# Kernel tuning notes

Measured on AMD Instinct MI355X. Metric: run time of the kernel, lower is better.

Reference implementation:

```python
import jax, jax.numpy as jnp
import numpy as np

B, C, D, H, W = 16, 8, 511, 16, 16
NHEADS = 16
DIM = C * H * W          # 2048 hidden size
SEQ = D + 1              # 512 tokens incl. cls
HEAD_DIM = DIM // NHEADS # 128


def setup_inputs() -> dict:
    key = jax.random.key(0)
    ks = jax.random.split(key, 8)
    s = 0.02  # weight init scale
    return {
        "x": jax.random.normal(ks[0], (B, C, D, H, W), jnp.float32),
        "pos_embedding": jax.random.normal(ks[1], (1, SEQ, DIM), jnp.float32),
        "cls": jax.random.normal(ks[2], (1, 1, DIM), jnp.float32),
        "qkv_w": jax.random.normal(ks[3], (DIM, 3 * DIM), jnp.float32) * s,
        "qkv_b": jnp.zeros((3 * DIM,), jnp.float32),
        "proj_w": jax.random.normal(ks[4], (DIM, DIM), jnp.float32) * s,
        "proj_b": jnp.zeros((DIM,), jnp.float32),
    }


def reference(x, pos_embedding, cls, qkv_w, qkv_b, proj_w, proj_b):
    b = x.shape[0]
    # rearrange 'b c d h w -> b d (c h w)'
    tok = jnp.transpose(x, (0, 2, 1, 3, 4)).reshape(b, D, DIM)
    tok = jnp.concatenate([jnp.broadcast_to(cls, (b, 1, DIM)), tok], axis=1)
    tok = tok + pos_embedding  # (b, SEQ, DIM)
    # qkv projection (dropout probs are 0 -> identity)
    qkv = tok @ qkv_w + qkv_b  # (b, SEQ, 3*DIM)
    qkv = qkv.reshape(b, SEQ, 3, NHEADS, HEAD_DIM).transpose(2, 0, 3, 1, 4)
    q, k, v = qkv[0], qkv[1], qkv[2]  # each (b, nH, SEQ, hd)
    scale = HEAD_DIM ** -0.5
    score = jax.nn.softmax(jnp.einsum('bhqd,bhkd->bhqk', q, k) * scale, axis=-1)
    out = jnp.einsum('bhqk,bhkd->bhqd', score, v)
    out = out.transpose(0, 2, 1, 3).reshape(b, SEQ, DIM)
    out = out @ proj_w + proj_b
    return out[:, 0]  # cls token, (b, DIM)
```

## Files before the change

### kernel.cpp

```cpp
#include <hip/hip_runtime.h>


#define BB   16
#define CC   8
#define DD   511
#define DIM  2048
#define SEQ  512
#define NH   16
#define HD   128
#define W3   6144
#define SCALE 0.08838834764831845f

#define Q_OFF   0
#define AO_OFF  2048
#define R_OFF   34816
#define G_OFF   67584
#define SC_OFF  67600
#define U8_OFF  198672

typedef __attribute__((ext_vector_type(8))) short short8;
typedef __attribute__((ext_vector_type(4))) float floatx4;

static __device__ inline short f2bf(float f) {
  union { float f; unsigned u; } v; v.f = f;
  unsigned r = v.u + 0x7fffu + ((v.u >> 16) & 1u);
  return (short)(r >> 16);
}
static __device__ inline float bf2f(short s) {
  union { unsigned u; float f; } v;
  v.u = ((unsigned)(unsigned short)s) << 16;
  return v.f;
}

__global__ __launch_bounds__(256) void k1_q(
    const float* __restrict__ pos, const float* __restrict__ cls,
    const float* __restrict__ qkv_w, const float* __restrict__ qkv_b,
    float* __restrict__ ws) {
  int n  = blockIdx.x * 256 + threadIdx.x;
  int d0 = blockIdx.y * 32;
  float acc = (blockIdx.y == 0) ? qkv_b[n] : 0.f;
#pragma unroll 8
  for (int d = d0; d < d0 + 32; ++d) {
    float t0 = cls[d] + pos[d];
    acc += t0 * qkv_w[(size_t)d * W3 + n];
  }
  atomicAdd(&ws[Q_OFF + n], acc);
}

__global__ __launch_bounds__(256) void k2_r(
    const float* __restrict__ qkv_w, float* __restrict__ ws) {
  __shared__ float qs[64];
  int h = blockIdx.y, ec = blockIdx.z;
  int d = blockIdx.x * 256 + threadIdx.x;
  if (threadIdx.x < 64) qs[threadIdx.x] = ws[Q_OFF + h * HD + ec * 64 + threadIdx.x];
  __syncthreads();
  const float4* w4 = reinterpret_cast<const float4*>(
      qkv_w + (size_t)d * W3 + DIM + h * HD + ec * 64);
  float acc = 0.f;
#pragma unroll
  for (int e4 = 0; e4 < 16; ++e4) {
    float4 w = w4[e4];
    acc += qs[e4*4+0]*w.x + qs[e4*4+1]*w.y + qs[e4*4+2]*w.z + qs[e4*4+3]*w.w;
  }
  atomicAdd(&ws[R_OFF + h * DIM + d], acc * SCALE);
}

__global__ __launch_bounds__(256) void k2b_gamma(
    const float* __restrict__ pos, const float* __restrict__ cls,
    float* __restrict__ ws) {
  __shared__ float red[256];
  int h = blockIdx.x, t = threadIdx.x;
  float part = 0.f;
  for (int d = t; d < DIM; d += 256)
    part += (cls[d] + pos[d]) * ws[R_OFF + h * DIM + d];
  red[t] = part;
  __syncthreads();
  for (int s = 128; s > 0; s >>= 1) {
    if (t < s) red[t] += red[t + s];
    __syncthreads();
  }
  if (t == 0) ws[G_OFF + h] = red[0];
}

__global__ __launch_bounds__(256) void k2c_rbf(float* __restrict__ ws) {
  int i = blockIdx.x * 256 + threadIdx.x;
  float v = ws[R_OFF + i];
  short hi = f2bf(v);
  short lo = f2bf(v - bf2f(hi));
  short* rb = (short*)(ws + U8_OFF);
  rb[i] = hi;
  rb[NH * DIM + i] = lo;
}

__global__ __launch_bounds__(64) void k3_scores_mfma(
    const float* __restrict__ x, const float* __restrict__ pos,
    float* __restrict__ ws) {
  int jt = blockIdx.x, b = blockIdx.y, ks = blockIdx.z;
  int l  = threadIdx.x;
  int m  = l & 15;
  int kg = l >> 4;
  int jrow = 1 + jt * 16 + m;
  int jc = jrow < SEQ ? jrow : (SEQ - 1);
  const size_t xrow = (size_t)b * CC * DD * 256 + (size_t)(jc - 1) * 256;
  const short* rh = (const short*)(ws + U8_OFF);
  const short* rl = rh + NH * DIM;
  floatx4 acc = {0.f, 0.f, 0.f, 0.f};
#pragma unroll 2
  for (int kk = ks * 32; kk < ks * 32 + 32; ++kk) {
    int d0 = kk * 32 + kg * 8;
    int c = d0 >> 8, doff = d0 & 255;
    const float4* xp = reinterpret_cast<const float4*>(
        x + xrow + (size_t)c * DD * 256 + doff);
    const float4* pp = reinterpret_cast<const float4*>(
        pos + (size_t)jc * DIM + d0);
    float4 xa = xp[0], xb = xp[1];
    float4 pa = pp[0], pb = pp[1];
    float f[8] = {xa.x + pa.x, xa.y + pa.y, xa.z + pa.z, xa.w + pa.w,
                  xb.x + pb.x, xb.y + pb.y, xb.z + pb.z, xb.w + pb.w};
    short8 ahi, alo;
#pragma unroll
    for (int i = 0; i < 8; ++i) {
      short hi = f2bf(f[i]);
      ahi[i] = hi;
      alo[i] = f2bf(f[i] - bf2f(hi));
    }
    short8 bhi = *reinterpret_cast<const short8*>(rh + m * DIM + d0);
    short8 blo = *reinterpret_cast<const short8*>(rl + m * DIM + d0);
    acc = __builtin_amdgcn_mfma_f32_16x16x32_bf16(ahi, bhi, acc, 0, 0, 0);
    acc = __builtin_amdgcn_mfma_f32_16x16x32_bf16(ahi, blo, acc, 0, 0, 0);
    acc = __builtin_amdgcn_mfma_f32_16x16x32_bf16(alo, bhi, acc, 0, 0, 0);
  }
  int h = m;
#pragma unroll
  for (int reg = 0; reg < 4; ++reg) {
    int row = kg * 4 + reg;
    int j = 1 + jt * 16 + row;
    if (j < SEQ)
      atomicAdd(&ws[SC_OFF + (size_t)(b * NH + h) * SEQ + j], acc[reg]);
  }
}

__global__ __launch_bounds__(256) void k4_softmax(float* __restrict__ ws) {
  int h = blockIdx.x, b = blockIdx.y, t = threadIdx.x;
  float* sc = ws + SC_OFF + (size_t)(b * NH + h) * SEQ;
  __shared__ float red[256];
  float s0 = (t == 0) ? ws[G_OFF + h] : sc[t];
  float s1 = sc[t + 256];
  red[t] = fmaxf(s0, s1);
  __syncthreads();
  for (int s = 128; s > 0; s >>= 1) { if (t < s) red[t] = fmaxf(red[t], red[t + s]); __syncthreads(); }
  float m = red[0];
  __syncthreads();
  float e0 = __expf(s0 - m), e1 = __expf(s1 - m);
  red[t] = e0 + e1;
  __syncthreads();
  for (int s = 128; s > 0; s >>= 1) { if (t < s) red[t] += red[t + s]; __syncthreads(); }
  float inv = 1.f / red[0];
  sc[t] = e0 * inv;
  sc[t + 256] = e1 * inv;
}

__global__ __launch_bounds__(256) void k5_u(
    const float* __restrict__ x, const float* __restrict__ pos,
    const float* __restrict__ cls, float* __restrict__ ws) {
  int c = blockIdx.x, qc = blockIdx.y, b = blockIdx.z, t = threadIdx.x;
  int d = c * 256 + t;
  __shared__ float pl[NH][64];
  __shared__ float pl0[NH];
  const float* pp = ws + SC_OFF + (size_t)b * NH * SEQ;
  int j0 = 1 + qc * 64;
  for (int i = t; i < NH * 64; i += 256) {
    int h = i >> 6, jj = i & 63;
    int j = j0 + jj;
    pl[h][jj] = (j < SEQ) ? pp[h * SEQ + j] : 0.f;
  }
  if (t < NH) pl0[t] = pp[t * SEQ];
  __syncthreads();
  float acc[NH];
  if (qc == 0) {
    float t0 = cls[d] + pos[d];
#pragma unroll
    for (int h = 0; h < NH; ++h) acc[h] = pl0[h] * t0;
  } else {
#pragma unroll
    for (int h = 0; h < NH; ++h) acc[h] = 0.f;
  }
  const size_t xb = (size_t)b * CC * DD * 256 + (size_t)c * DD * 256 + t;
  const float* posc = pos + c * 256 + t;
#pragma unroll 2
  for (int jt = 0; jt < 64; jt += 4) {
    float xvv[4];
#pragma unroll
    for (int jj = 0; jj < 4; ++jj) {
      int j = j0 + jt + jj;
      xvv[jj] = (j < SEQ)
          ? x[xb + (size_t)(j - 1) * 256] + posc[(size_t)j * DIM]
          : 0.f;
    }
#pragma unroll
    for (int h = 0; h < NH; ++h) {
      float4 p4 = *reinterpret_cast<const float4*>(&pl[h][jt]);
      acc[h] += p4.x * xvv[0] + p4.y * xvv[1] + p4.z * xvv[2] + p4.w * xvv[3];
    }
  }
  float* u = ws + U8_OFF + (size_t)((qc * BB + b) * NH) * DIM + d;
#pragma unroll
  for (int h = 0; h < NH; ++h) u[(size_t)h * DIM] = acc[h];
}

__global__ __launch_bounds__(256) void k6_ao(
    const float* __restrict__ qkv_w, const float* __restrict__ qkv_b,
    float* __restrict__ ws) {
  int nt = blockIdx.x, dc = blockIdx.y, t = threadIdx.x;
  int m = nt * 256 + t;
  int h0 = nt * 2;
  int d0 = dc * 64;
  __shared__ float us[2][64][20];
  for (int i = t; i < 2 * 64 * BB; i += 256) {
    int dd = i & 63, b = (i >> 6) & 15, hh = i >> 10;
    float s = 0.f;
#pragma unroll
    for (int q = 0; q < 8; ++q)
      s += ws[U8_OFF + (size_t)((q * BB + b) * NH + h0 + hh) * DIM + d0 + dd];
    us[hh][dd][b] = s;
  }
  __syncthreads();
  int hl = t >> 7;
  float acc[BB];
#pragma unroll
  for (int b = 0; b < BB; ++b) acc[b] = 0.f;
  const float* wcol = qkv_w + (size_t)d0 * W3 + 2 * DIM + m;
#pragma unroll 4
  for (int dd = 0; dd < 64; ++dd) {
    float w = wcol[(size_t)dd * W3];
    const float4* u4 = reinterpret_cast<const float4*>(&us[hl][dd][0]);
    float4 u0 = u4[0], u1 = u4[1], u2 = u4[2], u3 = u4[3];
    acc[0]  += u0.x * w; acc[1]  += u0.y * w; acc[2]  += u0.z * w; acc[3]  += u0.w * w;
    acc[4]  += u1.x * w; acc[5]  += u1.y * w; acc[6]  += u1.z * w; acc[7]  += u1.w * w;
    acc[8]  += u2.x * w; acc[9]  += u2.y * w; acc[10] += u2.z * w; acc[11] += u2.w * w;
    acc[12] += u3.x * w; acc[13] += u3.y * w; acc[14] += u3.z * w; acc[15] += u3.w * w;
  }
  float bias = (dc == 0) ? qkv_b[2 * DIM + m] : 0.f;
#pragma unroll
  for (int b = 0; b < BB; ++b)
    atomicAdd(&ws[AO_OFF + b * DIM + m], acc[b] + bias);
}

__global__ __launch_bounds__(256) void k7_out(
    const float* __restrict__ proj_w, const float* __restrict__ proj_b,
    const float* __restrict__ ws, float* __restrict__ out) {
  int nt = blockIdx.x, mc = blockIdx.y, t = threadIdx.x;
  int n = nt * 256 + t;
  int m0 = mc * 64;
  __shared__ float as[64][20];
  for (int i = t; i < 64 * BB; i += 256) {
    int mm = i & 63, b = i >> 6;
    as[mm][b] = ws[AO_OFF + b * DIM + m0 + mm];
  }
  __syncthreads();
  float acc[BB];
#pragma unroll
  for (int b = 0; b < BB; ++b) acc[b] = 0.f;
  const float* wcol = proj_w + (size_t)m0 * DIM + n;
#pragma unroll 4
  for (int mm = 0; mm < 64; ++mm) {
    float w = wcol[(size_t)mm * DIM];
    const float4* a4 = reinterpret_cast<const float4*>(&as[mm][0]);
    float4 a0 = a4[0], a1 = a4[1], a2 = a4[2], a3 = a4[3];
    acc[0]  += a0.x * w; acc[1]  += a0.y * w; acc[2]  += a0.z * w; acc[3]  += a0.w * w;
    acc[4]  += a1.x * w; acc[5]  += a1.y * w; acc[6]  += a1.z * w; acc[7]  += a1.w * w;
    acc[8]  += a2.x * w; acc[9]  += a2.y * w; acc[10] += a2.z * w; acc[11] += a2.w * w;
    acc[12] += a3.x * w; acc[13] += a3.y * w; acc[14] += a3.z * w; acc[15] += a3.w * w;
  }
  float bias = (mc == 0) ? proj_b[n] : 0.f;
#pragma unroll
  for (int b = 0; b < BB; ++b)
    atomicAdd(&out[b * DIM + n], acc[b] + bias);
}

extern "C" void kernel_launch(void* const* d_in, const int* in_sizes, int n_in,
                              void* d_out, int out_size, void* d_ws, size_t ws_size,
                              hipStream_t stream) {
  const float* x      = (const float*)d_in[0];
  const float* pos    = (const float*)d_in[1];
  const float* cls    = (const float*)d_in[2];
  const float* qkv_w  = (const float*)d_in[3];
  const float* qkv_b  = (const float*)d_in[4];
  const float* proj_w = (const float*)d_in[5];
  const float* proj_b = (const float*)d_in[6];
  float* ws  = (float*)d_ws;
  float* out = (float*)d_out;

  hipMemsetAsync(ws, 0, (size_t)(SC_OFF + 131072) * sizeof(float), stream);
  hipMemsetAsync(out, 0, (size_t)out_size * sizeof(float), stream);

  k1_q          <<<dim3(8, 64),     256, 0, stream>>>(pos, cls, qkv_w, qkv_b, ws);
  k2_r          <<<dim3(8, 16, 2),  256, 0, stream>>>(qkv_w, ws);
  k2b_gamma     <<<16,              256, 0, stream>>>(pos, cls, ws);
  k2c_rbf       <<<128,             256, 0, stream>>>(ws);
  k3_scores_mfma<<<dim3(32, 16, 2),  64, 0, stream>>>(x, pos, ws);
  k4_softmax    <<<dim3(16, 16),    256, 0, stream>>>(ws);
  k5_u          <<<dim3(8, 8, 16),  256, 0, stream>>>(x, pos, cls, ws);
  k6_ao         <<<dim3(8, 32),     256, 0, stream>>>(qkv_w, qkv_b, ws);
  k7_out        <<<dim3(8, 32),     256, 0, stream>>>(proj_w, proj_b, ws, out);
}
```

Before: 246.4 us.

## Fuse bf16 split into k2_r, atomically reduce U, and split GEMV K-dim finer

Folds the separate bf16 hi/lo conversion kernel into k2_r, which now covers the full head dimension per thread and writes R directly instead of using atomics. Rounding bf16 conversion is replaced by truncation. k5_u now accumulates partial U with atomics instead of storing eight partial slices that k6_ao later summed. k3, k6 and k7 split their reduction dimension finer to launch more blocks. The aim is fewer launches, less workspace traffic and more parallelism, at the cost of more atomics, a larger memset and slightly different rounding.

```diff
diff --git a/kernel.cpp b/kernel.cpp
--- a/kernel.cpp
+++ b/kernel.cpp
@@ -16,20 +16,17 @@
 #define R_OFF   34816
 #define G_OFF   67584
 #define SC_OFF  67600
-#define U8_OFF  198672
+#define U_OFF   198672
+#define RB_OFF  722960
 
 typedef __attribute__((ext_vector_type(8))) short short8;
 typedef __attribute__((ext_vector_type(4))) float floatx4;
 
-static __device__ inline short f2bf(float f) {
-  union { float f; unsigned u; } v; v.f = f;
-  unsigned r = v.u + 0x7fffu + ((v.u >> 16) & 1u);
-  return (short)(r >> 16);
-}
-static __device__ inline float bf2f(short s) {
-  union { unsigned u; float f; } v;
-  v.u = ((unsigned)(unsigned short)s) << 16;
-  return v.f;
+static __device__ inline short bf_hi(float f) {
+  return (short)(__float_as_uint(f) >> 16);
+}
+static __device__ inline float bf_hif(float f) {
+  return __uint_as_float(__float_as_uint(f) & 0xffff0000u);
 }
 
 __global__ __launch_bounds__(256) void k1_q(
@@ -47,22 +44,28 @@
   atomicAdd(&ws[Q_OFF + n], acc);
 }
 
-__global__ __launch_bounds__(256) void k2_r(
+__global__ __launch_bounds__(128) void k2_r(
     const float* __restrict__ qkv_w, float* __restrict__ ws) {
-  __shared__ float qs[64];
-  int h = blockIdx.y, ec = blockIdx.z;
-  int d = blockIdx.x * 256 + threadIdx.x;
-  if (threadIdx.x < 64) qs[threadIdx.x] = ws[Q_OFF + h * HD + ec * 64 + threadIdx.x];
+  __shared__ float qs[HD];
+  int h = blockIdx.y;
+  int d = blockIdx.x * 128 + threadIdx.x;
+  if (threadIdx.x < HD) qs[threadIdx.x] = ws[Q_OFF + h * HD + threadIdx.x];
   __syncthreads();
   const float4* w4 = reinterpret_cast<const float4*>(
-      qkv_w + (size_t)d * W3 + DIM + h * HD + ec * 64);
+      qkv_w + (size_t)d * W3 + DIM + h * HD);
   float acc = 0.f;
-#pragma unroll
-  for (int e4 = 0; e4 < 16; ++e4) {
+#pragma unroll 8
+  for (int e4 = 0; e4 < 32; ++e4) {
     float4 w = w4[e4];
     acc += qs[e4*4+0]*w.x + qs[e4*4+1]*w.y + qs[e4*4+2]*w.z + qs[e4*4+3]*w.w;
   }
-  atomicAdd(&ws[R_OFF + h * DIM + d], acc * SCALE);
+  float r = acc * SCALE;
+  int i = h * DIM + d;
+  ws[R_OFF + i] = r;
+  short* rb = (short*)(ws + RB_OFF);
+  short hi = bf_hi(r);
+  rb[i] = hi;
+  rb[NH * DIM + i] = bf_hi(r - bf_hif(r));
 }
 
 __global__ __launch_bounds__(256) void k2b_gamma(
@@ -80,16 +83,6 @@
     __syncthreads();
   }
   if (t == 0) ws[G_OFF + h] = red[0];
-}
-
-__global__ __launch_bounds__(256) void k2c_rbf(float* __restrict__ ws) {
-  int i = blockIdx.x * 256 + threadIdx.x;
-  float v = ws[R_OFF + i];
-  short hi = f2bf(v);
-  short lo = f2bf(v - bf2f(hi));
-  short* rb = (short*)(ws + U8_OFF);
-  rb[i] = hi;
-  rb[NH * DIM + i] = lo;
 }
 
 __global__ __launch_bounds__(64) void k3_scores_mfma(
@@ -102,11 +95,11 @@
   int jrow = 1 + jt * 16 + m;
   int jc = jrow < SEQ ? jrow : (SEQ - 1);
   const size_t xrow = (size_t)b * CC * DD * 256 + (size_t)(jc - 1) * 256;
-  const short* rh = (const short*)(ws + U8_OFF);
+  const short* rh = (const short*)(ws + RB_OFF);
   const short* rl = rh + NH * DIM;
   floatx4 acc = {0.f, 0.f, 0.f, 0.f};
 #pragma unroll 2
-  for (int kk = ks * 32; kk < ks * 32 + 32; ++kk) {
+  for (int kk = ks * 16; kk < ks * 16 + 16; ++kk) {
     int d0 = kk * 32 + kg * 8;
     int c = d0 >> 8, doff = d0 & 255;
     const float4* xp = reinterpret_cast<const float4*>(
@@ -120,9 +113,8 @@
     short8 ahi, alo;
 #pragma unroll
     for (int i = 0; i < 8; ++i) {
-      short hi = f2bf(f[i]);
-      ahi[i] = hi;
-      alo[i] = f2bf(f[i] - bf2f(hi));
+      ahi[i] = bf_hi(f[i]);
+      alo[i] = bf_hi(f[i] - bf_hif(f[i]));
     }
     short8 bhi = *reinterpret_cast<const short8*>(rh + m * DIM + d0);
     short8 blo = *reinterpret_cast<const short8*>(rl + m * DIM + d0);
@@ -203,9 +195,9 @@
       acc[h] += p4.x * xvv[0] + p4.y * xvv[1] + p4.z * xvv[2] + p4.w * xvv[3];
     }
   }
-  float* u = ws + U8_OFF + (size_t)((qc * BB + b) * NH) * DIM + d;
-#pragma unroll
-  for (int h = 0; h < NH; ++h) u[(size_t)h * DIM] = acc[h];
+  float* u = ws + U_OFF + (size_t)(b * NH) * DIM + d;
+#pragma unroll
+  for (int h = 0; h < NH; ++h) atomicAdd(&u[(size_t)h * DIM], acc[h]);
 }
 
 __global__ __launch_bounds__(256) void k6_ao(
@@ -214,15 +206,11 @@
   int nt = blockIdx.x, dc = blockIdx.y, t = threadIdx.x;
   int m = nt * 256 + t;
   int h0 = nt * 2;
-  int d0 = dc * 64;
-  __shared__ float us[2][64][20];
-  for (int i = t; i < 2 * 64 * BB; i += 256) {
-    int dd = i & 63, b = (i >> 6) & 15, hh = i >> 10;
-    float s = 0.f;
-#pragma unroll
-    for (int q = 0; q < 8; ++q)
-      s += ws[U8_OFF + (size_t)((q * BB + b) * NH + h0 + hh) * DIM + d0 + dd];
-    us[hh][dd][b] = s;
+  int d0 = dc * 32;
+  __shared__ float us[2][32][20];
+  for (int i = t; i < 2 * 32 * BB; i += 256) {
+    int dd = i & 31, b = (i >> 5) & 15, hh = i >> 9;
+    us[hh][dd][b] = ws[U_OFF + (size_t)(b * NH + h0 + hh) * DIM + d0 + dd];
   }
   __syncthreads();
   int hl = t >> 7;
@@ -231,7 +219,7 @@
   for (int b = 0; b < BB; ++b) acc[b] = 0.f;
   const float* wcol = qkv_w + (size_t)d0 * W3 + 2 * DIM + m;
 #pragma unroll 4
-  for (int dd = 0; dd < 64; ++dd) {
+  for (int dd = 0; dd < 32; ++dd) {
     float w = wcol[(size_t)dd * W3];
     const float4* u4 = reinterpret_cast<const float4*>(&us[hl][dd][0]);
     float4 u0 = u4[0], u1 = u4[1], u2 = u4[2], u3 = u4[3];
@@ -251,10 +239,10 @@
     const float* __restrict__ ws, float* __restrict__ out) {
   int nt = blockIdx.x, mc = blockIdx.y, t = threadIdx.x;
   int n = nt * 256 + t;
-  int m0 = mc * 64;
-  __shared__ float as[64][20];
-  for (int i = t; i < 64 * BB; i += 256) {
-    int mm = i & 63, b = i >> 6;
+  int m0 = mc * 32;
+  __shared__ float as[32][20];
+  for (int i = t; i < 32 * BB; i += 256) {
+    int mm = i & 31, b = i >> 5;
     as[mm][b] = ws[AO_OFF + b * DIM + m0 + mm];
   }
   __syncthreads();
@@ -263,7 +251,7 @@
   for (int b = 0; b < BB; ++b) acc[b] = 0.f;
   const float* wcol = proj_w + (size_t)m0 * DIM + n;
 #pragma unroll 4
-  for (int mm = 0; mm < 64; ++mm) {
+  for (int mm = 0; mm < 32; ++mm) {
     float w = wcol[(size_t)mm * DIM];
     const float4* a4 = reinterpret_cast<const float4*>(&as[mm][0]);
     float4 a0 = a4[0], a1 = a4[1], a2 = a4[2], a3 = a4[3];
@@ -291,16 +279,15 @@
   float* ws  = (float*)d_ws;
   float* out = (float*)d_out;
 
-  hipMemsetAsync(ws, 0, (size_t)(SC_OFF + 131072) * sizeof(float), stream);
+  hipMemsetAsync(ws, 0, (size_t)RB_OFF * sizeof(float), stream);
   hipMemsetAsync(out, 0, (size_t)out_size * sizeof(float), stream);
 
   k1_q          <<<dim3(8, 64),     256, 0, stream>>>(pos, cls, qkv_w, qkv_b, ws);
-  k2_r          <<<dim3(8, 16, 2),  256, 0, stream>>>(qkv_w, ws);
+  k2_r          <<<dim3(16, 16),    128, 0, stream>>>(qkv_w, ws);
   k2b_gamma     <<<16,              256, 0, stream>>>(pos, cls, ws);
-  k2c_rbf       <<<128,             256, 0, stream>>>(ws);
-  k3_scores_mfma<<<dim3(32, 16, 2),  64, 0, stream>>>(x, pos, ws);
+  k3_scores_mfma<<<dim3(32, 16, 4),  64, 0, stream>>>(x, pos, ws);
   k4_softmax    <<<dim3(16, 16),    256, 0, stream>>>(ws);
   k5_u          <<<dim3(8, 8, 16),  256, 0, stream>>>(x, pos, cls, ws);
-  k6_ao         <<<dim3(8, 32),     256, 0, stream>>>(qkv_w, qkv_b, ws);
-  k7_out        <<<dim3(8, 32),     256, 0, stream>>>(proj_w, proj_b, ws, out);
-}
+  k6_ao         <<<dim3(8, 64),     256, 0, stream>>>(qkv_w, qkv_b, ws);
+  k7_out        <<<dim3(8, 64),     256, 0, stream>>>(proj_w, proj_b, ws, out);
+}
```

Result: no change. 248.9 us (+1.0%).
